# Kernel tuning notes

Hardware: AMD Instinct MI355X
Metric: run time of the kernel (lower is better)

The kernel has to match this reference:

```python
import jax, jax.numpy as jnp
import numpy as np

B, S, E, H = 2, 2048, 1024, 16
HD = E // H


def setup_inputs() -> dict:
    key = jax.random.key(0)
    ks = jax.random.split(key, 5)
    scale = 1.0 / np.sqrt(E)
    return {
        "x": jax.random.normal(ks[0], (B, S, E), dtype=jnp.float32),
        "Wq": jax.random.normal(ks[1], (H, HD, E), dtype=jnp.float32) * scale,
        "Wk": jax.random.normal(ks[2], (H, HD, E), dtype=jnp.float32) * scale,
        "Wv": jax.random.normal(ks[3], (H, HD, E), dtype=jnp.float32) * scale,
        "Wo": jax.random.normal(ks[4], (E, E), dtype=jnp.float32) * scale,
    }


def reference(x, Wq, Wk, Wv, Wo):
    # Batched per-head projections: torch Linear y = x @ W.T, W: [head_dim, E]
    q = jnp.einsum("bse,hde->bshd", x, Wq)  # [B,S,H,HD]
    k = jnp.einsum("bse,hde->bshd", x, Wk)
    v = jnp.einsum("bse,hde->bshd", x, Wv)
    # Scaled dot-product attention; original scales by sqrt(head_dim)
    scores = jnp.einsum("bqhd,bkhd->bhqk", q, k) / jnp.sqrt(jnp.float32(HD))
    attn = jax.nn.softmax(scores, axis=-1)  # [B,H,S,S]
    out_h = jnp.einsum("bhqk,bkhd->bqhd", attn, v)  # [B,S,H,HD]
    out_cat = out_h.reshape(x.shape[0], x.shape[1], -1)  # concat heads -> [B,S,E]
    return out_cat @ Wo.T
```

## Files before the change

### kernel.cpp

```cpp
#include <hip/hip_runtime.h>
#include <hip/hip_bf16.h>

typedef unsigned short u16;
typedef unsigned int u32;
typedef __attribute__((ext_vector_type(4))) float f32x4;
typedef __attribute__((ext_vector_type(8))) short short8;
typedef __attribute__((ext_vector_type(8))) unsigned short u16x8;
typedef __attribute__((ext_vector_type(4))) unsigned short u16x4;
typedef __attribute__((ext_vector_type(2))) unsigned int u32x2;

#define BATCH 2
#define SEQ   2048
#define EMB   1024
#define NH    16
#define HD    64

__device__ inline u16 f2bf(float f) {
    unsigned u = __builtin_bit_cast(unsigned, f);
    unsigned r = u + 0x7FFFu + ((u >> 16) & 1u);
    return (u16)(r >> 16);
}

__device__ inline void gload16(const void* g, void* l) {
    __builtin_amdgcn_global_load_lds(
        (const __attribute__((address_space(1))) unsigned int*)g,
        (__attribute__((address_space(3))) unsigned int*)l, 16, 0, 0);
}

__global__ __launch_bounds__(256) void convert_all(
    const float* __restrict__ x,
    const float* __restrict__ Wq, const float* __restrict__ Wk, const float* __restrict__ Wv,
    u16* __restrict__ Xb, u16* __restrict__ Wqkv)
{
    const long gidx = (long)blockIdx.x * 2048 + (long)threadIdx.x * 8;
    const float* src;
    u16* dst;
    if (gidx < 4194304L) {
        src = x + gidx; dst = Xb + gidx;
    } else {
        const long r = gidx - 4194304L;
        const int w = (int)(r >> 20);
        const long off = r & 1048575L;
        src = (w == 0 ? Wq : w == 1 ? Wk : Wv) + off;
        dst = Wqkv + r;
    }
    f32x4 a = *(const f32x4*)src;
    f32x4 b = *(const f32x4*)(src + 4);
    u16x8 o;
    #pragma unroll
    for (int j = 0; j < 4; ++j) { o[j] = f2bf(a[j]); o[4 + j] = f2bf(b[j]); }
    *(u16x8*)dst = o;
}

__global__ __launch_bounds__(256) void convert_wo(
    const float* __restrict__ Wo, u16* __restrict__ Wob)
{
    const long gidx = (long)blockIdx.x * 2048 + (long)threadIdx.x * 8;
    f32x4 a = *(const f32x4*)(Wo + gidx);
    f32x4 b = *(const f32x4*)(Wo + gidx + 4);
    u16x8 o;
    #pragma unroll
    for (int j = 0; j < 4; ++j) { o[j] = f2bf(a[j]); o[4 + j] = f2bf(b[j]); }
    *(u16x8*)(Wob + gidx) = o;
}

template<int MODE>
__global__ __launch_bounds__(256) void gemm_bt(
    const u16* __restrict__ A, const u16* __restrict__ Bb,
    u16* __restrict__ Qo, u16* __restrict__ Ko, u16* __restrict__ VTo,
    float* __restrict__ Fo)
{
    __shared__ u16 As[128 * 64];
    __shared__ u16 Bs[128 * 64];

    const int tid = threadIdx.x;
    const int m0 = blockIdx.x * 128;
    const int n0 = blockIdx.y * 128;

    const int lane = tid & 63;
    const int lr = lane & 15;
    const int lg = lane >> 4;
    const int wid = tid >> 6;
    const int wm = wid >> 1, wn = wid & 1;

    const int grow = lane >> 3;
    const int gcolb = ((lane & 7) ^ grow) << 4;
    const int rswz = (lr & 7);

    f32x4 acc[4][4] = {};

    for (int kt = 0; kt < 16; ++kt) {
        const int k0b = kt * 128;
        __syncthreads();
        #pragma unroll
        for (int t = 0; t < 4; ++t) {
            const int row = (wid * 4 + t) * 8 + grow;
            gload16((const char*)A + (size_t)(m0 + row) * 2048 + k0b + gcolb,
                    (char*)As + (wid * 4 + t) * 1024);
            gload16((const char*)Bb + (size_t)(n0 + row) * 2048 + k0b + gcolb,
                    (char*)Bs + (wid * 4 + t) * 1024);
        }
        __syncthreads();

        #pragma unroll
        for (int kk = 0; kk < 2; ++kk) {
            short8 a[4], b[4];
            #pragma unroll
            for (int i = 0; i < 4; ++i)
                a[i] = *(const short8*)((const char*)As + (wm * 64 + i * 16 + lr) * 128
                                        + (((kk * 4 + lg) ^ rswz) << 4));
            #pragma unroll
            for (int i = 0; i < 4; ++i)
                b[i] = *(const short8*)((const char*)Bs + (wn * 64 + i * 16 + lr) * 128
                                        + (((kk * 4 + lg) ^ rswz) << 4));
            #pragma unroll
            for (int mi = 0; mi < 4; ++mi)
                #pragma unroll
                for (int ni = 0; ni < 4; ++ni)
                    acc[mi][ni] = __builtin_amdgcn_mfma_f32_16x16x32_bf16(a[mi], b[ni], acc[mi][ni], 0, 0, 0);
        }
    }

    const int mb = m0 + wm * 64;
    const int nb = n0 + wn * 64;
    if (MODE == 0) {
        const int w = n0 >> 10;
        const float qs = (w == 0) ? 0.125f : 1.0f;
        #pragma unroll
        for (int mi = 0; mi < 4; ++mi) {
            #pragma unroll
            for (int ni = 0; ni < 4; ++ni) {
                const int m = mb + mi * 16 + lg * 4;
                const int nn = (nb + ni * 16 + lr) & 1023;
                const int h = nn >> 6, d = nn & 63;
                const int bb = m >> 11, s = m & 2047;
                const size_t bh = (size_t)(bb * NH + h);
                if (w == 2) {
                    u16x4 v;
                    #pragma unroll
                    for (int i = 0; i < 4; ++i) v[i] = f2bf(acc[mi][ni][i]);
                    *(u16x4*)&VTo[(bh * HD + d) * SEQ + s] = v;
                } else {
                    u16* P = (w == 0) ? Qo : Ko;
                    #pragma unroll
                    for (int i = 0; i < 4; ++i)
                        P[(bh * SEQ + s + i) * HD + d] = f2bf(acc[mi][ni][i] * qs);
                }
            }
        }
    } else {
        #pragma unroll
        for (int mi = 0; mi < 4; ++mi)
            #pragma unroll
            for (int ni = 0; ni < 4; ++ni) {
                const int m = mb + mi * 16 + lg * 4;
                const int n = nb + ni * 16 + lr;
                #pragma unroll
                for (int i = 0; i < 4; ++i)
                    Fo[(size_t)(m + i) * EMB + n] = acc[mi][ni][i];
            }
    }
}

__global__ __launch_bounds__(512) void attn_fwd(
    const u16* __restrict__ Q, const u16* __restrict__ K,
    const u16* __restrict__ VT, u16* __restrict__ Cat)
{
    __shared__ u16 Ks[64 * 64];
    __shared__ u16 Vs[80 * 64];
    __shared__ u16 PT[8][16 * 72];

    const int tid = threadIdx.x;
    const int lane = tid & 63;
    const int lr = lane & 15;
    const int lg = lane >> 4;
    const int wid = tid >> 6;
    const int qt = blockIdx.x;
    const int bh = blockIdx.y;
    const int b = bh >> 4, h = bh & 15;

    if (tid < 128) {
        const int row = 64 + (tid >> 3), sl = tid & 7;
        u16x8 ones;
        #pragma unroll
        for (int j = 0; j < 8; ++j) ones[j] = 0x3F80;
        *(u16x8*)((char*)Vs + row * 128 + ((sl ^ (row & 7)) << 4)) = ones;
    }

    const u16* Qg = Q + ((size_t)bh * SEQ + qt * 128 + wid * 16 + lr) * HD;
    short8 qf[2];
    qf[0] = *(const short8*)(Qg + lg * 8);
    qf[1] = *(const short8*)(Qg + 32 + lg * 8);

    float m = -1e30f;
    f32x4 accO[5] = {};

    const u16* Kg = K + (size_t)bh * SEQ * HD;
    const u16* Vg = VT + (size_t)bh * HD * SEQ;

    const int srow = tid >> 3;
    const int scol = tid & 7;
    const int sswz = (scol ^ (srow & 7)) << 4;
    const u16* kp = Kg + (size_t)srow * HD + scol * 8;
    const u16* vp = Vg + (size_t)srow * SEQ + scol * 8;

    u16x8 kreg = *(const u16x8*)kp;
    u16x8 vreg = *(const u16x8*)vp;

    for (int nt = 0; nt < SEQ / 64; ++nt) {
        __syncthreads();
        *(u16x8*)((char*)Ks + srow * 128 + sswz) = kreg;
        *(u16x8*)((char*)Vs + srow * 128 + sswz) = vreg;
        if (nt + 1 < SEQ / 64) {
            kreg = *(const u16x8*)(kp + (size_t)(nt + 1) * 64 * HD);
            vreg = *(const u16x8*)(vp + (nt + 1) * 64);
        }
        __syncthreads();

        f32x4 st[4] = {};
        #pragma unroll
        for (int kk = 0; kk < 2; ++kk) {
            const short8 qv = qf[kk];
            #pragma unroll
            for (int c = 0; c < 4; ++c) {
                const short8 kf = *(const short8*)((const char*)Ks + (c * 16 + lr) * 128
                                                   + (((kk * 4 + lg) ^ (lr & 7)) << 4));
                st[c] = __builtin_amdgcn_mfma_f32_16x16x32_bf16(kf, qv, st[c], 0, 0, 0);
            }
        }

        float mx = fmaxf(
            fmaxf(fmaxf(fmaxf(st[0][0], st[0][1]), fmaxf(st[0][2], st[0][3])),
                  fmaxf(fmaxf(st[1][0], st[1][1]), fmaxf(st[1][2], st[1][3]))),
            fmaxf(fmaxf(fmaxf(st[2][0], st[2][1]), fmaxf(st[2][2], st[2][3])),
                  fmaxf(fmaxf(st[3][0], st[3][1]), fmaxf(st[3][2], st[3][3]))));
        mx = fmaxf(mx, __shfl_xor(mx, 16));
        mx = fmaxf(mx, __shfl_xor(mx, 32));
        if (!__all(mx - m <= 8.f)) {
            const float nm = fmaxf(m, mx);
            const float corr = __expf(m - nm);
            m = nm;
            #pragma unroll
            for (int dc = 0; dc < 5; ++dc)
                accO[dc] *= corr;
        }
        #pragma unroll
        for (int c = 0; c < 4; ++c)
            #pragma unroll
            for (int i = 0; i < 4; ++i)
                st[c][i] = __expf(st[c][i] - m);

        #pragma unroll
        for (int c = 0; c < 4; ++c) {
            u32 w0, w1;
            asm("v_cvt_pk_bf16_f32 %0, %1, %2" : "=v"(w0) : "v"(st[c][0]), "v"(st[c][1]));
            asm("v_cvt_pk_bf16_f32 %0, %1, %2" : "=v"(w1) : "v"(st[c][2]), "v"(st[c][3]));
            u32x2 pk; pk[0] = w0; pk[1] = w1;
            *(u32x2*)&PT[wid][lr * 72 + c * 16 + lg * 4] = pk;
        }
        asm volatile("s_waitcnt lgkmcnt(0)" ::: "memory");
        __builtin_amdgcn_sched_barrier(0);

        #pragma unroll
        for (int kk = 0; kk < 2; ++kk) {
            const short8 pf = *(const short8*)&PT[wid][lr * 72 + kk * 32 + lg * 8];
            #pragma unroll
            for (int dc = 0; dc < 5; ++dc) {
                const short8 vf = *(const short8*)((const char*)Vs + (dc * 16 + lr) * 128
                                                   + (((kk * 4 + lg) ^ (lr & 7)) << 4));
                accO[dc] = __builtin_amdgcn_mfma_f32_16x16x32_bf16(vf, pf, accO[dc], 0, 0, 0);
            }
        }
    }

    const float invl = 1.f / accO[4][0];
    const int qs = qt * 128 + wid * 16 + lr;
    u16* ob = Cat + (size_t)b * SEQ * EMB + (size_t)qs * EMB + h * HD;
    #pragma unroll
    for (int dc = 0; dc < 4; ++dc) {
        u16x4 o;
        #pragma unroll
        for (int i = 0; i < 4; ++i) o[i] = f2bf(accO[dc][i] * invl);
        *(u16x4*)&ob[dc * 16 + lg * 4] = o;
    }
}

extern "C" void kernel_launch(void* const* d_in, const int* in_sizes, int n_in,
                              void* d_out, int out_size, void* d_ws, size_t ws_size,
                              hipStream_t stream) {
    const float* x  = (const float*)d_in[0];
    const float* Wq = (const float*)d_in[1];
    const float* Wk = (const float*)d_in[2];
    const float* Wv = (const float*)d_in[3];
    const float* Wo = (const float*)d_in[4];
    float* out = (float*)d_out;

    u16* Xb   = (u16*)d_out;
    u16* Wqkv = (u16*)d_out + (size_t)4 * 1048576;

    char* ws = (char*)d_ws;
    u16* Qb  = (u16*)(ws);
    u16* Kb  = (u16*)(ws + (size_t)8  * 1048576);
    u16* VTb = (u16*)(ws + (size_t)16 * 1048576);
    u16* Cat = (u16*)(ws + (size_t)24 * 1048576);
    u16* Wob = Qb;

    convert_all<<<3584, 256, 0, stream>>>(x, Wq, Wk, Wv, Xb, Wqkv);

    dim3 g1(4096 / 128, 3072 / 128);
    gemm_bt<0><<<g1, 256, 0, stream>>>(Xb, Wqkv, Qb, Kb, VTb, nullptr);

    dim3 g2(SEQ / 128, BATCH * NH);
    attn_fwd<<<g2, 512, 0, stream>>>(Qb, Kb, VTb, Cat);

    convert_wo<<<512, 256, 0, stream>>>(Wo, Wob);
    dim3 g3(4096 / 128, 1024 / 128);
    gemm_bt<1><<<g3, 256, 0, stream>>>(Cat, Wob, nullptr, nullptr, nullptr, out);
}
```

Before: 132.5 us.

## Double-buffer LDS tiles with direct global-to-LDS loads; switch softmax to exp2

```diff
diff --git a/kernel.cpp b/kernel.cpp
--- a/kernel.cpp
+++ b/kernel.cpp
@@ -19,6 +19,12 @@
     unsigned u = __builtin_bit_cast(unsigned, f);
     unsigned r = u + 0x7FFFu + ((u >> 16) & 1u);
     return (u16)(r >> 16);
+}
+
+__device__ inline float fexp2(float x) {
+    float r;
+    asm("v_exp_f32 %0, %1" : "=v"(r) : "v"(x));
+    return r;
 }
 
 __device__ inline void gload16(const void* g, void* l) {
@@ -70,8 +76,8 @@
     u16* __restrict__ Qo, u16* __restrict__ Ko, u16* __restrict__ VTo,
     float* __restrict__ Fo)
 {
-    __shared__ u16 As[128 * 64];
-    __shared__ u16 Bs[128 * 64];
+    __shared__ u16 As[2][128 * 64];
+    __shared__ u16 Bs[2][128 * 64];
 
     const int tid = threadIdx.x;
     const int m0 = blockIdx.x * 128;
@@ -89,29 +95,37 @@
 
     f32x4 acc[4][4] = {};
 
-    for (int kt = 0; kt < 16; ++kt) {
+    auto issue = [&](int kt, int buf) {
         const int k0b = kt * 128;
-        __syncthreads();
         #pragma unroll
         for (int t = 0; t < 4; ++t) {
             const int row = (wid * 4 + t) * 8 + grow;
             gload16((const char*)A + (size_t)(m0 + row) * 2048 + k0b + gcolb,
-                    (char*)As + (wid * 4 + t) * 1024);
+                    (char*)As[buf] + (wid * 4 + t) * 1024);
             gload16((const char*)Bb + (size_t)(n0 + row) * 2048 + k0b + gcolb,
-                    (char*)Bs + (wid * 4 + t) * 1024);
-        }
+                    (char*)Bs[buf] + (wid * 4 + t) * 1024);
+        }
+    };
+
+    issue(0, 0);
+
+    for (int kt = 0; kt < 16; ++kt) {
+        const int cur = kt & 1;
         __syncthreads();
-
+        if (kt + 1 < 16) issue(kt + 1, cur ^ 1);
+
+        const u16* Ac = As[cur];
+        const u16* Bc = Bs[cur];
         #pragma unroll
         for (int kk = 0; kk < 2; ++kk) {
             short8 a[4], b[4];
             #pragma unroll
             for (int i = 0; i < 4; ++i)
-                a[i] = *(const short8*)((const char*)As + (wm * 64 + i * 16 + lr) * 128
+                a[i] = *(const short8*)((const char*)Ac + (wm * 64 + i * 16 + lr) * 128
                                         + (((kk * 4 + lg) ^ rswz) << 4));
             #pragma unroll
             for (int i = 0; i < 4; ++i)
-                b[i] = *(const short8*)((const char*)Bs + (wn * 64 + i * 16 + lr) * 128
+                b[i] = *(const short8*)((const char*)Bc + (wn * 64 + i * 16 + lr) * 128
                                         + (((kk * 4 + lg) ^ rswz) << 4));
             #pragma unroll
             for (int mi = 0; mi < 4; ++mi)
@@ -125,7 +139,7 @@
     const int nb = n0 + wn * 64;
     if (MODE == 0) {
         const int w = n0 >> 10;
-        const float qs = (w == 0) ? 0.125f : 1.0f;
+        const float qs = (w == 0) ? 0.125f * 1.44269504f : 1.0f;
         #pragma unroll
         for (int mi = 0; mi < 4; ++mi) {
             #pragma unroll
@@ -166,8 +180,8 @@
     const u16* __restrict__ Q, const u16* __restrict__ K,
     const u16* __restrict__ VT, u16* __restrict__ Cat)
 {
-    __shared__ u16 Ks[64 * 64];
-    __shared__ u16 Vs[80 * 64];
+    __shared__ u16 Ks[2][64 * 64];
+    __shared__ u16 Vs[2][80 * 64];
     __shared__ u16 PT[8][16 * 72];
 
     const int tid = threadIdx.x;
@@ -184,7 +198,8 @@
         u16x8 ones;
         #pragma unroll
         for (int j = 0; j < 8; ++j) ones[j] = 0x3F80;
-        *(u16x8*)((char*)Vs + row * 128 + ((sl ^ (row & 7)) << 4)) = ones;
+        *(u16x8*)((char*)Vs[0] + row * 128 + ((sl ^ (row & 7)) << 4)) = ones;
+        *(u16x8*)((char*)Vs[1] + row * 128 + ((sl ^ (row & 7)) << 4)) = ones;
     }
 
     const u16* Qg = Q + ((size_t)bh * SEQ + qt * 128 + wid * 16 + lr) * HD;
@@ -198,24 +213,24 @@
     const u16* Kg = K + (size_t)bh * SEQ * HD;
     const u16* Vg = VT + (size_t)bh * HD * SEQ;
 
-    const int srow = tid >> 3;
-    const int scol = tid & 7;
-    const int sswz = (scol ^ (srow & 7)) << 4;
-    const u16* kp = Kg + (size_t)srow * HD + scol * 8;
-    const u16* vp = Vg + (size_t)srow * SEQ + scol * 8;
-
-    u16x8 kreg = *(const u16x8*)kp;
-    u16x8 vreg = *(const u16x8*)vp;
+    const int srow = lane >> 3;
+    const int schunk = ((lane & 7) ^ srow) << 4;
+
+    auto issueKV = [&](int nt, int buf) {
+        const int kv0 = nt * 64;
+        const int krow = wid * 8 + srow;
+        gload16((const char*)Kg + (size_t)(kv0 + krow) * 128 + schunk,
+                (char*)Ks[buf] + wid * 1024);
+        gload16((const char*)Vg + (size_t)krow * (SEQ * 2) + kv0 * 2 + schunk,
+                (char*)Vs[buf] + wid * 1024);
+    };
+
+    issueKV(0, 0);
 
     for (int nt = 0; nt < SEQ / 64; ++nt) {
+        const int cur = nt & 1;
         __syncthreads();
-        *(u16x8*)((char*)Ks + srow * 128 + sswz) = kreg;
-        *(u16x8*)((char*)Vs + srow * 128 + sswz) = vreg;
-        if (nt + 1 < SEQ / 64) {
-            kreg = *(const u16x8*)(kp + (size_t)(nt + 1) * 64 * HD);
-            vreg = *(const u16x8*)(vp + (nt + 1) * 64);
-        }
-        __syncthreads();
+        if (nt + 1 < SEQ / 64) issueKV(nt + 1, cur ^ 1);
 
         f32x4 st[4] = {};
         #pragma unroll
@@ -223,7 +238,7 @@
             const short8 qv = qf[kk];
             #pragma unroll
             for (int c = 0; c < 4; ++c) {
-                const short8 kf = *(const short8*)((const char*)Ks + (c * 16 + lr) * 128
+                const short8 kf = *(const short8*)((const char*)Ks[cur] + (c * 16 + lr) * 128
                                                    + (((kk * 4 + lg) ^ (lr & 7)) << 4));
                 st[c] = __builtin_amdgcn_mfma_f32_16x16x32_bf16(kf, qv, st[c], 0, 0, 0);
             }
@@ -236,9 +251,9 @@
                   fmaxf(fmaxf(st[3][0], st[3][1]), fmaxf(st[3][2], st[3][3]))));
         mx = fmaxf(mx, __shfl_xor(mx, 16));
         mx = fmaxf(mx, __shfl_xor(mx, 32));
-        if (!__all(mx - m <= 8.f)) {
+        if (!__all(mx - m <= 11.5f)) {
             const float nm = fmaxf(m, mx);
-            const float corr = __expf(m - nm);
+            const float corr = fexp2(m - nm);
             m = nm;
             #pragma unroll
             for (int dc = 0; dc < 5; ++dc)
@@ -248,7 +263,7 @@
         for (int c = 0; c < 4; ++c)
             #pragma unroll
             for (int i = 0; i < 4; ++i)
-                st[c][i] = __expf(st[c][i] - m);
+                st[c][i] = fexp2(st[c][i] - m);
 
         #pragma unroll
         for (int c = 0; c < 4; ++c) {
@@ -266,7 +281,7 @@
             const short8 pf = *(const short8*)&PT[wid][lr * 72 + kk * 32 + lg * 8];
             #pragma unroll
             for (int dc = 0; dc < 5; ++dc) {
-                const short8 vf = *(const short8*)((const char*)Vs + (dc * 16 + lr) * 128
+                const short8 vf = *(const short8*)((const char*)Vs[cur] + (dc * 16 + lr) * 128
                                                    + (((kk * 4 + lg) ^ (lr & 7)) << 4));
                 accO[dc] = __builtin_amdgcn_mfma_f32_16x16x32_bf16(vf, pf, accO[dc], 0, 0, 0);
             }
```

Result: no change. 130.4 us (-1.5%).
